# Performance work log

Measured on AMD Instinct MI355X. Metric: run time of the kernel, lower is better.

The kernel has to match this reference:

```python
import jax, jax.numpy as jnp
import numpy as np
import math

D_MODEL = 1024
NUM_HEADS = 16
D_K = D_MODEL // NUM_HEADS
THETA = 10000.0
NEG_INF = 1.0e6  # module uses -1e6, not -inf


def _rope_tables(seq_len):
    pair_idx = jnp.arange(0, D_K, 2, dtype=jnp.float32)
    inv_freq = 1.0 / (THETA ** (pair_idx / D_K))
    pos = jnp.arange(seq_len, dtype=jnp.float32)
    angles = jnp.outer(pos, inv_freq)  # (S, D_K//2)
    return jnp.cos(angles), jnp.sin(angles)


def _apply_rope(x, cos, sin):
    # x: (B, H, S, D_K); cos/sin: (S, D_K//2)
    xe = x[..., 0::2]
    xo = x[..., 1::2]
    oe = xe * cos - xo * sin
    oo = xe * sin + xo * cos
    return jnp.stack([oe, oo], axis=-1).reshape(x.shape)


def setup_inputs() -> dict:
    key = jax.random.key(0)
    k0, k1, k2, k3, k4 = jax.random.split(key, 5)
    B, S = 2, 2048
    x = jax.random.normal(k0, (B, S, D_MODEL), dtype=jnp.float32)
    scale = 0.02
    wq = jax.random.normal(k1, (D_MODEL, D_MODEL), dtype=jnp.float32) * scale
    wk = jax.random.normal(k2, (D_MODEL, D_MODEL), dtype=jnp.float32) * scale
    wv = jax.random.normal(k3, (D_MODEL, D_MODEL), dtype=jnp.float32) * scale
    wo = jax.random.normal(k4, (D_MODEL, D_MODEL), dtype=jnp.float32) * scale
    return {"x": x, "wq": wq, "wk": wk, "wv": wv, "wo": wo}


def reference(x, wq, wk, wv, wo):
    B, S, _ = x.shape
    q = x @ wq.T
    k = x @ wk.T
    v = x @ wv.T
    # (B, S, H, d_k) -> (B, H, S, d_k)
    q = q.reshape(B, S, NUM_HEADS, D_K).transpose(0, 2, 1, 3)
    k = k.reshape(B, S, NUM_HEADS, D_K).transpose(0, 2, 1, 3)
    v = v.reshape(B, S, NUM_HEADS, D_K).transpose(0, 2, 1, 3)
    cos, sin = _rope_tables(S)
    q = _apply_rope(q, cos, sin)
    k = _apply_rope(k, cos, sin)
    scores = jnp.einsum("bhqd,bhkd->bhqk", q, k) / math.sqrt(D_K)
    causal = jnp.tril(jnp.ones((S, S), dtype=bool))
    scores = jnp.where(causal, scores, -NEG_INF)
    attn = jax.nn.softmax(scores, axis=-1)
    out = jnp.einsum("bhqk,bhkd->bhqd", attn, v)
    out = out.transpose(0, 2, 1, 3).reshape(B, S, D_MODEL)
    return out @ wo.T
```

## Files before the change

### kernel.cpp

```cpp
#include <hip/hip_runtime.h>

typedef __attribute__((ext_vector_type(8))) __bf16 bf16x8;
typedef __attribute__((ext_vector_type(8))) _Float16 f16x8;
typedef __attribute__((ext_vector_type(4))) _Float16 f16x4;
typedef __attribute__((ext_vector_type(4))) float f32x4;
typedef __attribute__((ext_vector_type(8))) unsigned short u16x8;
typedef __attribute__((ext_vector_type(4))) unsigned int u32x4;

#define MFMA_BF16(a, b, c) __builtin_amdgcn_mfma_f32_16x16x32_bf16((a), (b), (c), 0, 0, 0)
#define MFMA_F16(a, b, c)  __builtin_amdgcn_mfma_f32_16x16x32_f16((a), (b), (c), 0, 0, 0)
#define LOG2E 1.44269504088896340736f
#define QSCALE 0.18033688011112042f

__device__ __forceinline__ float b2f(unsigned short u) {
    union { unsigned int i; float f; } v; v.i = ((unsigned int)u) << 16; return v.f;
}
__device__ __forceinline__ unsigned short f2bf(float f) {
    union { float f; unsigned int i; } v; v.f = f;
    unsigned int u = v.i;
    return (unsigned short)((u + 0x7fffu + ((u >> 16) & 1u)) >> 16);
}

__device__ __forceinline__ void gl_lds16(const void* g, void* l) {
    __builtin_amdgcn_global_load_lds(
        (const __attribute__((address_space(1))) void*)g,
        (__attribute__((address_space(3))) void*)l,
        16, 0, 0);
}

__global__ __launch_bounds__(256) void cvt_all(const float* __restrict__ x,
                                               const float* __restrict__ wq,
                                               const float* __restrict__ wk,
                                               const float* __restrict__ wv,
                                               const float* __restrict__ wo,
                                               unsigned short* __restrict__ xb,
                                               unsigned short* __restrict__ wqb,
                                               unsigned short* __restrict__ wkb,
                                               unsigned short* __restrict__ wvb,
                                               unsigned short* __restrict__ wob) {
    int id = blockIdx.x * 256 + threadIdx.x;
    const float* src; unsigned short* dst; size_t off; float scl = 1.0f;
    if (id < 524288)      { src = x;  dst = xb;  off = (size_t)id * 8; }
    else if (id < 655360) { src = wq; dst = wqb; off = (size_t)(id - 524288) * 8; scl = QSCALE; }
    else if (id < 786432) { src = wk; dst = wkb; off = (size_t)(id - 655360) * 8; }
    else if (id < 917504) { src = wv; dst = wvb; off = (size_t)(id - 786432) * 8; }
    else                  { src = wo; dst = wob; off = (size_t)(id - 917504) * 8; }
    float4 a = *(const float4*)(src + off);
    float4 b = *(const float4*)(src + off + 4);
    u16x8 o;
    o[0] = f2bf(a.x * scl); o[1] = f2bf(a.y * scl); o[2] = f2bf(a.z * scl); o[3] = f2bf(a.w * scl);
    o[4] = f2bf(b.x * scl); o[5] = f2bf(b.y * scl); o[6] = f2bf(b.z * scl); o[7] = f2bf(b.w * scl);
    *(u16x8*)(dst + off) = o;
}

template <int MODE>
__device__ __forceinline__ void gemm128_bt(const unsigned short* __restrict__ A,
                                           const unsigned short* __restrict__ B,
                                           void* __restrict__ Cv,
                                           int m0, int n0, int ldc,
                                           unsigned short* As, unsigned short* Bs) {
    const int tid = threadIdx.x;
    const int w = tid >> 6, lane = tid & 63;
    const int quad = lane >> 4, l15 = lane & 15;
    const int wm = w & 1, wn = w >> 1;

    f32x4 acc[4][4];
#pragma unroll
    for (int mt = 0; mt < 4; ++mt)
#pragma unroll
        for (int nt = 0; nt < 4; ++nt) acc[mt][nt] = f32x4{0.f, 0.f, 0.f, 0.f};

    for (int k0 = 0; k0 < 1024; k0 += 32) {
        __syncthreads();
#pragma unroll
        for (int i = 0; i < 2; ++i) {
            int L = (w * 2 + i) * 64 + lane;
            int r = L >> 2;
            int c = (L & 3) ^ ((r >> 1) & 3);
            gl_lds16(A + (size_t)(m0 + r) * 1024 + k0 + c * 8, As + L * 8);
            gl_lds16(B + (size_t)(n0 + r) * 1024 + k0 + c * 8, Bs + L * 8);
        }
        __syncthreads();

        bf16x8 af[4], bfr[4];
#pragma unroll
        for (int mt = 0; mt < 4; ++mt) {
            int row = wm * 64 + mt * 16 + l15;
            af[mt] = *(const bf16x8*)(As + row * 32 + (quad ^ ((row >> 1) & 3)) * 8);
        }
#pragma unroll
        for (int nt = 0; nt < 4; ++nt) {
            int row = wn * 64 + nt * 16 + l15;
            bfr[nt] = *(const bf16x8*)(Bs + row * 32 + (quad ^ ((row >> 1) & 3)) * 8);
        }
#pragma unroll
        for (int mt = 0; mt < 4; ++mt)
#pragma unroll
            for (int nt = 0; nt < 4; ++nt)
                acc[mt][nt] = MFMA_BF16(af[mt], bfr[nt], acc[mt][nt]);
    }

    float invf[4], sgn = 0.f;
    if constexpr (MODE == 3) {
        sgn = (l15 & 1) ? 1.0f : -1.0f;
#pragma unroll
        for (int nt = 0; nt < 4; ++nt)
            invf[nt] = exp2f(-0.41524101186092029f * (float)((nt * 16 + l15) >> 1));
    }

#pragma unroll
    for (int mt = 0; mt < 4; ++mt) {
        int grow = m0 + wm * 64 + mt * 16 + quad * 4;
#pragma unroll
        for (int nt = 0; nt < 4; ++nt) {
            int gcol = n0 + wn * 64 + nt * 16 + l15;
#pragma unroll
            for (int r = 0; r < 4; ++r) {
                float val = acc[mt][nt][r];
                size_t idx = (size_t)(grow + r) * ldc + gcol;
                if constexpr (MODE == 0) {
                    ((unsigned short*)Cv)[idx] = f2bf(val);
                } else if constexpr (MODE == 1) {
                    ((float*)Cv)[idx] = val;
                } else if constexpr (MODE == 2) {
                    _Float16 hv = (_Float16)val;
                    ((unsigned short*)Cv)[idx] = __builtin_bit_cast(unsigned short, hv);
                } else {
                    float p = __shfl_xor(val, 1);
                    float pos = (float)((grow + r) & 2047);
                    float ang = pos * invf[nt];
                    float out = val * __cosf(ang) + sgn * p * __sinf(ang);
                    ((unsigned short*)Cv)[idx] = f2bf(out);
                }
            }
        }
    }
}

__global__ __launch_bounds__(256) void gemm_qkv(const unsigned short* __restrict__ X,
                                                const unsigned short* __restrict__ Wq,
                                                const unsigned short* __restrict__ Wk,
                                                const unsigned short* __restrict__ Wv,
                                                unsigned short* __restrict__ Qo,
                                                unsigned short* __restrict__ Ko,
                                                unsigned short* __restrict__ Vt) {
    __shared__ unsigned short As[128 * 32];
    __shared__ unsigned short Bs[128 * 32];
    int y = blockIdx.y;
    if (y < 16) {
        int sel = y >> 3;
        int m0 = blockIdx.x * 128;
        int n0 = (y & 7) * 128;
        const unsigned short* B = sel ? Wk : Wq;
        unsigned short* C = sel ? Ko : Qo;
        gemm128_bt<3>(X, B, C, m0, n0, 1024, As, Bs);
    } else {
        int m0 = (y & 7) * 128;
        int n0 = blockIdx.x * 128;
        gemm128_bt<2>(Wv, X, Vt, m0, n0, 4096, As, Bs);
    }
}

__global__ __launch_bounds__(256) void gemm_out(const unsigned short* __restrict__ A,
                                                const unsigned short* __restrict__ Wo,
                                                float* __restrict__ C) {
    __shared__ unsigned short As[128 * 32];
    __shared__ unsigned short Bs[128 * 32];
    gemm128_bt<1>(A, Wo, C, blockIdx.x * 128, blockIdx.y * 128, 1024, As, Bs);
}

#define FBODY(MASKED)                                                                   \
    {                                                                                   \
        bf16x8 kf[4][2];                                                                \
        _Pragma("unroll")                                                               \
        for (int nt = 0; nt < 4; ++nt) {                                                \
            int row = nt * 16 + l15;                                                    \
            const char* kp = (const char*)Ksb + row * 128;                              \
            int swk = row & 7;                                                          \
            kf[nt][0] = *(const bf16x8*)(kp + ((quad ^ swk) << 4));                     \
            kf[nt][1] = *(const bf16x8*)(kp + (((quad ^ 4) ^ swk) << 4));               \
        }                                                                               \
        f16x8 pf[2][2];                                                                 \
        _Pragma("unroll")                                                               \
        for (int mt = 0; mt < 2; ++mt) {                                                \
            f32x4 sc[4];                                                                \
            _Pragma("unroll")                                                           \
            for (int nt = 0; nt < 4; ++nt) {                                            \
                f32x4 z = f32x4{0.f, 0.f, 0.f, 0.f};                                    \
                z = MFMA_BF16(kf[nt][0], qf[mt][0], z);                                 \
                sc[nt] = MFMA_BF16(kf[nt][1], qf[mt][1], z);                            \
            }                                                                           \
            int qpos = qposw + mt * 16 + l15;                                           \
            unsigned pk[8];                                                             \
            _Pragma("unroll")                                                           \
            for (int nt = 0; nt < 4; ++nt) {                                            \
                float e[4];                                                             \
                _Pragma("unroll")                                                       \
                for (int r = 0; r < 4; ++r) {                                           \
                    float ev = exp2f(sc[nt][r]);                                        \
                    if (MASKED) {                                                       \
                        int kpos = kb * 64 + nt * 16 + quad * 4 + r;                    \
                        ev = (kpos > qpos) ? 0.f : ev;                                  \
                    }                                                                   \
                    e[r] = ev;                                                          \
                }                                                                       \
                pk[nt * 2 + 0] = __builtin_bit_cast(unsigned,                           \
                                     __builtin_amdgcn_cvt_pkrtz(e[0], e[1]));           \
                pk[nt * 2 + 1] = __builtin_bit_cast(unsigned,                           \
                                     __builtin_amdgcn_cvt_pkrtz(e[2], e[3]));           \
            }                                                                           \
            u32x4 pw0 = u32x4{pk[0], pk[1], pk[2], pk[3]};                              \
            u32x4 pw1 = u32x4{pk[4], pk[5], pk[6], pk[7]};                              \
            pf[mt][0] = __builtin_bit_cast(f16x8, pw0);                                 \
            pf[mt][1] = __builtin_bit_cast(f16x8, pw1);                                 \
            lacc[mt] = MFMA_F16(pf[mt][0], ones, lacc[mt]);                             \
            lacc[mt] = MFMA_F16(pf[mt][1], ones, lacc[mt]);                             \
        }                                                                               \
        _Pragma("unroll")                                                               \
        for (int nt = 0; nt < 4; ++nt) {                                                \
            int rowd = nt * 16 + l15;                                                   \
            const char* vp = (const char*)Vsb + rowd * 128;                             \
            int swv = rowd & 7;                                                         \
            int qh = quad >> 1, sub = (quad & 1) * 8;                                   \
            f16x4 a0 = *(const f16x4*)(vp + (((qh + 0) ^ swv) << 4) + sub);             \
            f16x4 a1 = *(const f16x4*)(vp + (((qh + 2) ^ swv) << 4) + sub);             \
            f16x8 v0 = __builtin_shufflevector(a0, a1, 0, 1, 2, 3, 4, 5, 6, 7);         \
            accO[0][nt] = MFMA_F16(pf[0][0], v0, accO[0][nt]);                          \
            accO[1][nt] = MFMA_F16(pf[1][0], v0, accO[1][nt]);                          \
            f16x4 b0 = *(const f16x4*)(vp + (((qh + 4) ^ swv) << 4) + sub);             \
            f16x4 b1 = *(const f16x4*)(vp + (((qh + 6) ^ swv) << 4) + sub);             \
            f16x8 v1 = __builtin_shufflevector(b0, b1, 0, 1, 2, 3, 4, 5, 6, 7);         \
            accO[0][nt] = MFMA_F16(pf[0][1], v1, accO[0][nt]);                          \
            accO[1][nt] = MFMA_F16(pf[1][1], v1, accO[1][nt]);                          \
        }                                                                               \
    }

__global__ __launch_bounds__(256) void flash_attn(const unsigned short* __restrict__ Q,
                                                  const unsigned short* __restrict__ Kb,
                                                  const unsigned short* __restrict__ Vt,
                                                  unsigned short* __restrict__ O) {
    int id = blockIdx.x;
    int xcd = id & 7;
    int sl = id >> 3;
    int rr = sl >> 3;
    int j  = sl & 7;
    int bh = xcd + 8 * rr;
    int b = bh >> 4, h = bh & 15;
    int tid = threadIdx.x, w = tid >> 6, lane = tid & 63;
    int quad = lane >> 4, l15 = lane & 15;

    __shared__ unsigned short Ks[2 * 4096];
    __shared__ unsigned short Vs[2 * 4096];

    int L0 = w * 128 + lane;
    int L1 = L0 + 64;
    int r0 = L0 >> 3, c0 = (L0 & 7) ^ (r0 & 7);
    int r1 = L1 >> 3, c1 = (L1 & 7) ^ (r1 & 7);
    const unsigned short* Kg0 = Kb + (size_t)(b * 2048 + r0) * 1024 + h * 64 + c0 * 8;
    const unsigned short* Kg1 = Kb + (size_t)(b * 2048 + r1) * 1024 + h * 64 + c1 * 8;
    const unsigned short* Vg0 = Vt + (size_t)(h * 64 + r0) * 4096 + b * 2048 + c0 * 8;
    const unsigned short* Vg1 = Vt + (size_t)(h * 64 + r1) * 4096 + b * 2048 + c1 * 8;

    f16x8 ones;
#pragma unroll
    for (int t = 0; t < 8; ++t) ones[t] = (_Float16)1.0f;

#define STAGE(kb_, buf_)                                                    \
    {                                                                       \
        size_t ko = (size_t)(kb_) * 64 * 1024;                              \
        size_t vo = (size_t)(kb_) * 64;                                     \
        unsigned short* kd = Ks + (buf_) * 4096;                            \
        unsigned short* vd = Vs + (buf_) * 4096;                            \
        gl_lds16(Kg0 + ko, kd + L0 * 8);                                    \
        gl_lds16(Kg1 + ko, kd + L1 * 8);                                    \
        gl_lds16(Vg0 + vo, vd + L0 * 8);                                    \
        gl_lds16(Vg1 + vo, vd + L1 * 8);                                    \
    }

    for (int tp = 0; tp < 2; ++tp) {
        int qt = tp ? (15 - j) : j;
        int qrow0 = b * 2048 + qt * 128 + w * 32;
        int qposw = qt * 128 + w * 32;
        int nkb = 2 * qt + 2;

        STAGE(0, 0)

        bf16x8 qf[2][2];
#pragma unroll
        for (int mt = 0; mt < 2; ++mt) {
            const unsigned short* qp =
                Q + (size_t)(qrow0 + mt * 16 + l15) * 1024 + h * 64 + quad * 8;
            qf[mt][0] = *(const bf16x8*)qp;
            qf[mt][1] = *(const bf16x8*)(qp + 32);
        }

        f32x4 accO[2][4];
        f32x4 lacc[2];
#pragma unroll
        for (int mt = 0; mt < 2; ++mt) {
            lacc[mt] = f32x4{0.f, 0.f, 0.f, 0.f};
#pragma unroll
            for (int nt = 0; nt < 4; ++nt) accO[mt][nt] = f32x4{0.f, 0.f, 0.f, 0.f};
        }

        __asm__ volatile("s_waitcnt vmcnt(0)" ::: "memory");
        __builtin_amdgcn_s_barrier();
        __builtin_amdgcn_sched_barrier(0);

        int cur = 0;
        for (int kb = 0; kb < nkb; ++kb) {
            if (kb + 1 < nkb) STAGE(kb + 1, cur ^ 1)
            const unsigned short* Ksb = Ks + cur * 4096;
            const unsigned short* Vsb = Vs + cur * 4096;
            if (kb < nkb - 2) {
                FBODY(0)
            } else {
                FBODY(1)
            }
            __asm__ volatile("s_waitcnt vmcnt(0)" ::: "memory");
            __builtin_amdgcn_s_barrier();
            __builtin_amdgcn_sched_barrier(0);
            cur ^= 1;
        }

#pragma unroll
        for (int mt = 0; mt < 2; ++mt) {
            float inv[4];
#pragma unroll
            for (int r = 0; r < 4; ++r) inv[r] = 1.0f / lacc[mt][r];
#pragma unroll
            for (int nt = 0; nt < 4; ++nt)
#pragma unroll
                for (int r = 0; r < 4; ++r)
                    O[(size_t)(qrow0 + mt * 16 + quad * 4 + r) * 1024 +
                      h * 64 + nt * 16 + l15] = f2bf(accO[mt][nt][r] * inv[r]);
        }
    }
#undef STAGE
}

extern "C" void kernel_launch(void* const* d_in, const int* in_sizes, int n_in,
                              void* d_out, int out_size, void* d_ws, size_t ws_size,
                              hipStream_t stream) {
    (void)in_sizes; (void)n_in; (void)out_size; (void)ws_size;
    const float* x  = (const float*)d_in[0];
    const float* wq = (const float*)d_in[1];
    const float* wk = (const float*)d_in[2];
    const float* wv = (const float*)d_in[3];
    const float* wo = (const float*)d_in[4];
    float* out = (float*)d_out;

    const size_t T = (size_t)4096 * 1024;
    const size_t W = (size_t)1024 * 1024;
    unsigned short* Q   = (unsigned short*)d_ws;
    unsigned short* K   = Q + T;
    unsigned short* Vt  = K + T;
    unsigned short* xb  = Vt + T;
    unsigned short* AO  = xb;
    unsigned short* wqb = xb + T;
    unsigned short* wkb = wqb + W;
    unsigned short* wvb = wkb + W;
    unsigned short* wob = wvb + W;

    cvt_all  <<<dim3(4096),   256, 0, stream>>>(x, wq, wk, wv, wo, xb, wqb, wkb, wvb, wob);
    gemm_qkv <<<dim3(32, 24), 256, 0, stream>>>(xb, wqb, wkb, wvb, Q, K, Vt);
    flash_attn<<<dim3(256),   256, 0, stream>>>(Q, K, Vt, AO);
    gemm_out <<<dim3(32, 8),  256, 0, stream>>>(AO, wob, out);
}
```

Baseline: 187.4 us.

## Split flash attention into one q-tile per block and swizzle P fragments

The attention kernel previously had each of 256 blocks process two paired query tiles (j and 15-j) one after another. It now launches 512 blocks, each handling a single query tile, with a causal-balanced ordering mapping t to qt. This is meant to improve occupancy and tail balance across CUs. Separately, the P operand is rearranged across lanes using ds_swizzle, so V fragments can be read from LDS as single 16-byte loads instead of two 8-byte loads plus a shuffle. The cost is extra swizzle instructions and more blocks, each with its own prologue and Q load.

```diff
diff --git a/kernel.cpp b/kernel.cpp
--- a/kernel.cpp
+++ b/kernel.cpp
@@ -2,7 +2,6 @@
 
 typedef __attribute__((ext_vector_type(8))) __bf16 bf16x8;
 typedef __attribute__((ext_vector_type(8))) _Float16 f16x8;
-typedef __attribute__((ext_vector_type(4))) _Float16 f16x4;
 typedef __attribute__((ext_vector_type(4))) float f32x4;
 typedef __attribute__((ext_vector_type(8))) unsigned short u16x8;
 typedef __attribute__((ext_vector_type(4))) unsigned int u32x4;
@@ -175,12 +174,12 @@
         _Pragma("unroll")                                                               \
         for (int nt = 0; nt < 4; ++nt) {                                                \
             int row = nt * 16 + l15;                                                    \
-            const char* kp = (const char*)Ksb + row * 128;                              \
+            const unsigned short* kp = Ksb + row * 64;                                  \
             int swk = row & 7;                                                          \
-            kf[nt][0] = *(const bf16x8*)(kp + ((quad ^ swk) << 4));                     \
-            kf[nt][1] = *(const bf16x8*)(kp + (((quad ^ 4) ^ swk) << 4));               \
+            kf[nt][0] = *(const bf16x8*)(kp + (quad ^ swk) * 8);                        \
+            kf[nt][1] = *(const bf16x8*)(kp + ((quad ^ 4) ^ swk) * 8);                  \
         }                                                                               \
-        f16x8 pf[2][2];                                                                 \
+        f16x8 pa[2][2];                                                                 \
         _Pragma("unroll")                                                               \
         for (int mt = 0; mt < 2; ++mt) {                                                \
             f32x4 sc[4];                                                                \
@@ -209,29 +208,37 @@
                 pk[nt * 2 + 1] = __builtin_bit_cast(unsigned,                           \
                                      __builtin_amdgcn_cvt_pkrtz(e[2], e[3]));           \
             }                                                                           \
-            u32x4 pw0 = u32x4{pk[0], pk[1], pk[2], pk[3]};                              \
-            u32x4 pw1 = u32x4{pk[4], pk[5], pk[6], pk[7]};                              \
-            pf[mt][0] = __builtin_bit_cast(f16x8, pw0);                                 \
-            pf[mt][1] = __builtin_bit_cast(f16x8, pw1);                                 \
-            lacc[mt] = MFMA_F16(pf[mt][0], ones, lacc[mt]);                             \
-            lacc[mt] = MFMA_F16(pf[mt][1], ones, lacc[mt]);                             \
+            u32x4 rs0 = u32x4{pk[0], pk[1], pk[2], pk[3]};                              \
+            u32x4 rs1 = u32x4{pk[4], pk[5], pk[6], pk[7]};                              \
+            lacc[mt] = MFMA_F16(__builtin_bit_cast(f16x8, rs0), ones, lacc[mt]);        \
+            lacc[mt] = MFMA_F16(__builtin_bit_cast(f16x8, rs1), ones, lacc[mt]);        \
+            int b0 = quad & 1;                                                          \
+            unsigned y0 = (unsigned)__builtin_amdgcn_ds_swizzle(                        \
+                              (int)(b0 ? pk[0] : pk[2]), 0x401F);                       \
+            unsigned y1 = (unsigned)__builtin_amdgcn_ds_swizzle(                        \
+                              (int)(b0 ? pk[1] : pk[3]), 0x401F);                       \
+            unsigned y2 = (unsigned)__builtin_amdgcn_ds_swizzle(                        \
+                              (int)(b0 ? pk[4] : pk[6]), 0x401F);                       \
+            unsigned y3 = (unsigned)__builtin_amdgcn_ds_swizzle(                        \
+                              (int)(b0 ? pk[5] : pk[7]), 0x401F);                       \
+            u32x4 t0 = b0 ? u32x4{y0, y1, pk[2], pk[3]}                                 \
+                          : u32x4{pk[0], pk[1], y0, y1};                                \
+            u32x4 t1 = b0 ? u32x4{y2, y3, pk[6], pk[7]}                                 \
+                          : u32x4{pk[4], pk[5], y2, y3};                                \
+            pa[mt][0] = __builtin_bit_cast(f16x8, t0);                                  \
+            pa[mt][1] = __builtin_bit_cast(f16x8, t1);                                  \
         }                                                                               \
         _Pragma("unroll")                                                               \
         for (int nt = 0; nt < 4; ++nt) {                                                \
             int rowd = nt * 16 + l15;                                                   \
-            const char* vp = (const char*)Vsb + rowd * 128;                             \
-            int swv = rowd & 7;                                                         \
-            int qh = quad >> 1, sub = (quad & 1) * 8;                                   \
-            f16x4 a0 = *(const f16x4*)(vp + (((qh + 0) ^ swv) << 4) + sub);             \
-            f16x4 a1 = *(const f16x4*)(vp + (((qh + 2) ^ swv) << 4) + sub);             \
-            f16x8 v0 = __builtin_shufflevector(a0, a1, 0, 1, 2, 3, 4, 5, 6, 7);         \
-            accO[0][nt] = MFMA_F16(pf[0][0], v0, accO[0][nt]);                          \
-            accO[1][nt] = MFMA_F16(pf[1][0], v0, accO[1][nt]);                          \
-            f16x4 b0 = *(const f16x4*)(vp + (((qh + 4) ^ swv) << 4) + sub);             \
-            f16x4 b1 = *(const f16x4*)(vp + (((qh + 6) ^ swv) << 4) + sub);             \
-            f16x8 v1 = __builtin_shufflevector(b0, b1, 0, 1, 2, 3, 4, 5, 6, 7);         \
-            accO[0][nt] = MFMA_F16(pf[0][1], v1, accO[0][nt]);                          \
-            accO[1][nt] = MFMA_F16(pf[1][1], v1, accO[1][nt]);                          \
+            const unsigned short* vp = Vsb + rowd * 64;                                 \
+            int sl0 = pi4 ^ (rowd & 7);                                                 \
+            f16x8 v0 = *(const f16x8*)(vp + sl0 * 8);                                   \
+            f16x8 v1 = *(const f16x8*)(vp + (sl0 ^ 4) * 8);                             \
+            accO[0][nt] = MFMA_F16(pa[0][0], v0, accO[0][nt]);                          \
+            accO[1][nt] = MFMA_F16(pa[1][0], v0, accO[1][nt]);                          \
+            accO[0][nt] = MFMA_F16(pa[0][1], v1, accO[0][nt]);                          \
+            accO[1][nt] = MFMA_F16(pa[1][1], v1, accO[1][nt]);                          \
         }                                                                               \
     }
 
@@ -241,13 +248,15 @@
                                                   unsigned short* __restrict__ O) {
     int id = blockIdx.x;
     int xcd = id & 7;
-    int sl = id >> 3;
-    int rr = sl >> 3;
-    int j  = sl & 7;
+    int s  = id >> 3;
+    int rr = s & 3;
+    int t  = s >> 2;
+    int qt = (t < 8) ? t : 23 - t;
     int bh = xcd + 8 * rr;
     int b = bh >> 4, h = bh & 15;
     int tid = threadIdx.x, w = tid >> 6, lane = tid & 63;
     int quad = lane >> 4, l15 = lane & 15;
+    int pi4 = ((quad & 1) << 1) | (quad >> 1);
 
     __shared__ unsigned short Ks[2 * 4096];
     __shared__ unsigned short Vs[2 * 4096];
@@ -263,7 +272,7 @@
 
     f16x8 ones;
 #pragma unroll
-    for (int t = 0; t < 8; ++t) ones[t] = (_Float16)1.0f;
+    for (int tt = 0; tt < 8; ++tt) ones[tt] = (_Float16)1.0f;
 
 #define STAGE(kb_, buf_)                                                    \
     {                                                                       \
@@ -277,64 +286,61 @@
         gl_lds16(Vg1 + vo, vd + L1 * 8);                                    \
     }
 
-    for (int tp = 0; tp < 2; ++tp) {
-        int qt = tp ? (15 - j) : j;
-        int qrow0 = b * 2048 + qt * 128 + w * 32;
-        int qposw = qt * 128 + w * 32;
-        int nkb = 2 * qt + 2;
-
-        STAGE(0, 0)
-
-        bf16x8 qf[2][2];
-#pragma unroll
-        for (int mt = 0; mt < 2; ++mt) {
-            const unsigned short* qp =
-                Q + (size_t)(qrow0 + mt * 16 + l15) * 1024 + h * 64 + quad * 8;
-            qf[mt][0] = *(const bf16x8*)qp;
-            qf[mt][1] = *(const bf16x8*)(qp + 32);
-        }
-
-        f32x4 accO[2][4];
-        f32x4 lacc[2];
-#pragma unroll
-        for (int mt = 0; mt < 2; ++mt) {
-            lacc[mt] = f32x4{0.f, 0.f, 0.f, 0.f};
-#pragma unroll
-            for (int nt = 0; nt < 4; ++nt) accO[mt][nt] = f32x4{0.f, 0.f, 0.f, 0.f};
-        }
-
+    int qrow0 = b * 2048 + qt * 128 + w * 32;
+    int qposw = qt * 128 + w * 32;
+    int nkb = 2 * qt + 2;
+
+    STAGE(0, 0)
+
+    bf16x8 qf[2][2];
+#pragma unroll
+    for (int mt = 0; mt < 2; ++mt) {
+        const unsigned short* qp =
+            Q + (size_t)(qrow0 + mt * 16 + l15) * 1024 + h * 64 + quad * 8;
+        qf[mt][0] = *(const bf16x8*)qp;
+        qf[mt][1] = *(const bf16x8*)(qp + 32);
+    }
+
+    f32x4 accO[2][4];
+    f32x4 lacc[2];
+#pragma unroll
+    for (int mt = 0; mt < 2; ++mt) {
+        lacc[mt] = f32x4{0.f, 0.f, 0.f, 0.f};
+#pragma unroll
+        for (int nt = 0; nt < 4; ++nt) accO[mt][nt] = f32x4{0.f, 0.f, 0.f, 0.f};
+    }
+
+    __asm__ volatile("s_waitcnt vmcnt(0)" ::: "memory");
+    __builtin_amdgcn_s_barrier();
+    __builtin_amdgcn_sched_barrier(0);
+
+    int cur = 0;
+    for (int kb = 0; kb < nkb; ++kb) {
+        if (kb + 1 < nkb) STAGE(kb + 1, cur ^ 1)
+        const unsigned short* Ksb = Ks + cur * 4096;
+        const unsigned short* Vsb = Vs + cur * 4096;
+        if (kb < nkb - 2) {
+            FBODY(0)
+        } else {
+            FBODY(1)
+        }
         __asm__ volatile("s_waitcnt vmcnt(0)" ::: "memory");
         __builtin_amdgcn_s_barrier();
         __builtin_amdgcn_sched_barrier(0);
-
-        int cur = 0;
-        for (int kb = 0; kb < nkb; ++kb) {
-            if (kb + 1 < nkb) STAGE(kb + 1, cur ^ 1)
-            const unsigned short* Ksb = Ks + cur * 4096;
-            const unsigned short* Vsb = Vs + cur * 4096;
-            if (kb < nkb - 2) {
-                FBODY(0)
-            } else {
-                FBODY(1)
-            }
-            __asm__ volatile("s_waitcnt vmcnt(0)" ::: "memory");
-            __builtin_amdgcn_s_barrier();
-            __builtin_amdgcn_sched_barrier(0);
-            cur ^= 1;
-        }
-
-#pragma unroll
-        for (int mt = 0; mt < 2; ++mt) {
-            float inv[4];
-#pragma unroll
-            for (int r = 0; r < 4; ++r) inv[r] = 1.0f / lacc[mt][r];
-#pragma unroll
-            for (int nt = 0; nt < 4; ++nt)
-#pragma unroll
-                for (int r = 0; r < 4; ++r)
-                    O[(size_t)(qrow0 + mt * 16 + quad * 4 + r) * 1024 +
-                      h * 64 + nt * 16 + l15] = f2bf(accO[mt][nt][r] * inv[r]);
-        }
+        cur ^= 1;
+    }
+
+#pragma unroll
+    for (int mt = 0; mt < 2; ++mt) {
+        float inv[4];
+#pragma unroll
+        for (int r = 0; r < 4; ++r) inv[r] = 1.0f / lacc[mt][r];
+#pragma unroll
+        for (int nt = 0; nt < 4; ++nt)
+#pragma unroll
+            for (int r = 0; r < 4; ++r)
+                O[(size_t)(qrow0 + mt * 16 + quad * 4 + r) * 1024 +
+                  h * 64 + nt * 16 + l15] = f2bf(accO[mt][nt][r] * inv[r]);
     }
 #undef STAGE
 }
@@ -364,6 +370,6 @@
 
     cvt_all  <<<dim3(4096),   256, 0, stream>>>(x, wq, wk, wv, wo, xb, wqb, wkb, wvb, wob);
     gemm_qkv <<<dim3(32, 24), 256, 0, stream>>>(xb, wqb, wkb, wvb, Q, K, Vt);
-    flash_attn<<<dim3(256),   256, 0, stream>>>(Q, K, Vt, AO);
+    flash_attn<<<dim3(512),   256, 0, stream>>>(Q, K, Vt, AO);
     gemm_out <<<dim3(32, 8),  256, 0, stream>>>(AO, wob, out);
 }
```

New measurement: 190.5 us. About the same (+1.7%).

## Load K/V directly into registers with single-wave blocks in flash attention

Applied to the files above, without the earlier changes.

Rewrites the attention kernel so that each 64-thread block handles one 32-row query slice. K and V fragments are loaded straight from global memory into registers with a two-deep software prefetch, replacing the LDS staging, the barriers and the paired causal-tile scheduling. Blocks are ordered so the longest query tiles launch first. The change removes LDS traffic and synchronization, but the global K/V reads are no longer shared across the waves of a block, so L2 and global bandwidth demand rises and register pressure grows.

```diff
diff --git a/kernel.cpp b/kernel.cpp
--- a/kernel.cpp
+++ b/kernel.cpp
@@ -169,26 +169,43 @@
     gemm128_bt<1>(A, Wo, C, blockIdx.x * 128, blockIdx.y * 128, 1024, As, Bs);
 }
 
-#define FBODY(MASKED)                                                                   \
+
+#define LOADK(DST, KB_)                                                     \
+    {                                                                       \
+        const unsigned short* kp_ = KgL + (size_t)(KB_) * 65536;            \
+        DST[0][0] = *(const bf16x8*)(kp_);                                  \
+        DST[0][1] = *(const bf16x8*)(kp_ + 32);                             \
+        DST[1][0] = *(const bf16x8*)(kp_ + 16384);                          \
+        DST[1][1] = *(const bf16x8*)(kp_ + 16384 + 32);                     \
+        DST[2][0] = *(const bf16x8*)(kp_ + 32768);                          \
+        DST[2][1] = *(const bf16x8*)(kp_ + 32768 + 32);                     \
+        DST[3][0] = *(const bf16x8*)(kp_ + 49152);                          \
+        DST[3][1] = *(const bf16x8*)(kp_ + 49152 + 32);                     \
+    }
+
+#define LOADV(DST, KB_)                                                     \
+    {                                                                       \
+        const unsigned short* vp_ = VgL + (size_t)(KB_) * 64;               \
+        _Pragma("unroll")                                                   \
+        for (int nt_ = 0; nt_ < 4; ++nt_) {                                 \
+            DST[nt_][0] = *(const f16x4*)(vp_ + nt_ * 65536);               \
+            DST[nt_][1] = *(const f16x4*)(vp_ + nt_ * 65536 + 16);          \
+            DST[nt_][2] = *(const f16x4*)(vp_ + nt_ * 65536 + 32);          \
+            DST[nt_][3] = *(const f16x4*)(vp_ + nt_ * 65536 + 48);          \
+        }                                                                   \
+    }
+
+#define FCOMP(KF, VP, KB_, MASKED)                                                      \
     {                                                                                   \
-        bf16x8 kf[4][2];                                                                \
-        _Pragma("unroll")                                                               \
-        for (int nt = 0; nt < 4; ++nt) {                                                \
-            int row = nt * 16 + l15;                                                    \
-            const char* kp = (const char*)Ksb + row * 128;                              \
-            int swk = row & 7;                                                          \
-            kf[nt][0] = *(const bf16x8*)(kp + ((quad ^ swk) << 4));                     \
-            kf[nt][1] = *(const bf16x8*)(kp + (((quad ^ 4) ^ swk) << 4));               \
-        }                                                                               \
-        f16x8 pf[2][2];                                                                 \
+        f16x8 paR[2][2];                                                                \
         _Pragma("unroll")                                                               \
         for (int mt = 0; mt < 2; ++mt) {                                                \
             f32x4 sc[4];                                                                \
             _Pragma("unroll")                                                           \
             for (int nt = 0; nt < 4; ++nt) {                                            \
                 f32x4 z = f32x4{0.f, 0.f, 0.f, 0.f};                                    \
-                z = MFMA_BF16(kf[nt][0], qf[mt][0], z);                                 \
-                sc[nt] = MFMA_BF16(kf[nt][1], qf[mt][1], z);                            \
+                z = MFMA_BF16(KF[nt][0], qf[mt][0], z);                                 \
+                sc[nt] = MFMA_BF16(KF[nt][1], qf[mt][1], z);                            \
             }                                                                           \
             int qpos = qposw + mt * 16 + l15;                                           \
             unsigned pk[8];                                                             \
@@ -199,7 +216,7 @@
                 for (int r = 0; r < 4; ++r) {                                           \
                     float ev = exp2f(sc[nt][r]);                                        \
                     if (MASKED) {                                                       \
-                        int kpos = kb * 64 + nt * 16 + quad * 4 + r;                    \
+                        int kpos = (KB_) * 64 + nt * 16 + quad * 4 + r;                 \
                         ev = (kpos > qpos) ? 0.f : ev;                                  \
                     }                                                                   \
                     e[r] = ev;                                                          \
@@ -209,134 +226,104 @@
                 pk[nt * 2 + 1] = __builtin_bit_cast(unsigned,                           \
                                      __builtin_amdgcn_cvt_pkrtz(e[2], e[3]));           \
             }                                                                           \
-            u32x4 pw0 = u32x4{pk[0], pk[1], pk[2], pk[3]};                              \
-            u32x4 pw1 = u32x4{pk[4], pk[5], pk[6], pk[7]};                              \
-            pf[mt][0] = __builtin_bit_cast(f16x8, pw0);                                 \
-            pf[mt][1] = __builtin_bit_cast(f16x8, pw1);                                 \
-            lacc[mt] = MFMA_F16(pf[mt][0], ones, lacc[mt]);                             \
-            lacc[mt] = MFMA_F16(pf[mt][1], ones, lacc[mt]);                             \
+            u32x4 w0 = u32x4{pk[0], pk[1], pk[2], pk[3]};                               \
+            u32x4 w1 = u32x4{pk[4], pk[5], pk[6], pk[7]};                               \
+            f16x8 pa0 = __builtin_bit_cast(f16x8, w0);                                  \
+            f16x8 pa1 = __builtin_bit_cast(f16x8, w1);                                  \
+            lacc[mt] = MFMA_F16(pa0, ones, lacc[mt]);                                   \
+            lacc[mt] = MFMA_F16(pa1, ones, lacc[mt]);                                   \
+            paR[mt][0] = pa0;                                                           \
+            paR[mt][1] = pa1;                                                           \
         }                                                                               \
         _Pragma("unroll")                                                               \
         for (int nt = 0; nt < 4; ++nt) {                                                \
-            int rowd = nt * 16 + l15;                                                   \
-            const char* vp = (const char*)Vsb + rowd * 128;                             \
-            int swv = rowd & 7;                                                         \
-            int qh = quad >> 1, sub = (quad & 1) * 8;                                   \
-            f16x4 a0 = *(const f16x4*)(vp + (((qh + 0) ^ swv) << 4) + sub);             \
-            f16x4 a1 = *(const f16x4*)(vp + (((qh + 2) ^ swv) << 4) + sub);             \
-            f16x8 v0 = __builtin_shufflevector(a0, a1, 0, 1, 2, 3, 4, 5, 6, 7);         \
-            accO[0][nt] = MFMA_F16(pf[0][0], v0, accO[0][nt]);                          \
-            accO[1][nt] = MFMA_F16(pf[1][0], v0, accO[1][nt]);                          \
-            f16x4 b0 = *(const f16x4*)(vp + (((qh + 4) ^ swv) << 4) + sub);             \
-            f16x4 b1 = *(const f16x4*)(vp + (((qh + 6) ^ swv) << 4) + sub);             \
-            f16x8 v1 = __builtin_shufflevector(b0, b1, 0, 1, 2, 3, 4, 5, 6, 7);         \
-            accO[0][nt] = MFMA_F16(pf[0][1], v1, accO[0][nt]);                          \
-            accO[1][nt] = MFMA_F16(pf[1][1], v1, accO[1][nt]);                          \
+            f16x8 v0 = __builtin_shufflevector(VP[nt][0], VP[nt][1],                    \
+                                               0, 1, 2, 3, 4, 5, 6, 7);                 \
+            f16x8 v1 = __builtin_shufflevector(VP[nt][2], VP[nt][3],                    \
+                                               0, 1, 2, 3, 4, 5, 6, 7);                 \
+            accO[0][nt] = MFMA_F16(paR[0][0], v0, accO[0][nt]);                         \
+            accO[1][nt] = MFMA_F16(paR[1][0], v0, accO[1][nt]);                         \
+            accO[0][nt] = MFMA_F16(paR[0][1], v1, accO[0][nt]);                         \
+            accO[1][nt] = MFMA_F16(paR[1][1], v1, accO[1][nt]);                         \
         }                                                                               \
     }
 
-__global__ __launch_bounds__(256) void flash_attn(const unsigned short* __restrict__ Q,
-                                                  const unsigned short* __restrict__ Kb,
-                                                  const unsigned short* __restrict__ Vt,
-                                                  unsigned short* __restrict__ O) {
+__global__ __launch_bounds__(64, 2) void flash_attn(const unsigned short* __restrict__ Q,
+                                                    const unsigned short* __restrict__ Kb,
+                                                    const unsigned short* __restrict__ Vt,
+                                                    unsigned short* __restrict__ O) {
     int id = blockIdx.x;
     int xcd = id & 7;
-    int sl = id >> 3;
-    int rr = sl >> 3;
-    int j  = sl & 7;
+    int idx = id >> 3;
+    int rr = idx & 3;
+    int w  = (idx >> 2) & 3;
+    int qt = 15 - (idx >> 4);
     int bh = xcd + 8 * rr;
     int b = bh >> 4, h = bh & 15;
-    int tid = threadIdx.x, w = tid >> 6, lane = tid & 63;
+    int lane = threadIdx.x & 63;
     int quad = lane >> 4, l15 = lane & 15;
 
-    __shared__ unsigned short Ks[2 * 4096];
-    __shared__ unsigned short Vs[2 * 4096];
-
-    int L0 = w * 128 + lane;
-    int L1 = L0 + 64;
-    int r0 = L0 >> 3, c0 = (L0 & 7) ^ (r0 & 7);
-    int r1 = L1 >> 3, c1 = (L1 & 7) ^ (r1 & 7);
-    const unsigned short* Kg0 = Kb + (size_t)(b * 2048 + r0) * 1024 + h * 64 + c0 * 8;
-    const unsigned short* Kg1 = Kb + (size_t)(b * 2048 + r1) * 1024 + h * 64 + c1 * 8;
-    const unsigned short* Vg0 = Vt + (size_t)(h * 64 + r0) * 4096 + b * 2048 + c0 * 8;
-    const unsigned short* Vg1 = Vt + (size_t)(h * 64 + r1) * 4096 + b * 2048 + c1 * 8;
+    int qrow0 = b * 2048 + qt * 128 + w * 32;
+    int qposw = qt * 128 + w * 32;
+    int nkb = 2 * qt + 2;
+
+    const unsigned short* KgL = Kb + (size_t)(b * 2048 + l15) * 1024 + h * 64 + quad * 8;
+    const unsigned short* VgL = Vt + (size_t)(h * 64 + l15) * 4096 + b * 2048 + quad * 4;
+
+    bf16x8 qf[2][2];
+#pragma unroll
+    for (int mt = 0; mt < 2; ++mt) {
+        const unsigned short* qp =
+            Q + (size_t)(qrow0 + mt * 16 + l15) * 1024 + h * 64 + quad * 8;
+        qf[mt][0] = *(const bf16x8*)qp;
+        qf[mt][1] = *(const bf16x8*)(qp + 32);
+    }
 
     f16x8 ones;
 #pragma unroll
-    for (int t = 0; t < 8; ++t) ones[t] = (_Float16)1.0f;
-
-#define STAGE(kb_, buf_)                                                    \
-    {                                                                       \
-        size_t ko = (size_t)(kb_) * 64 * 1024;                              \
-        size_t vo = (size_t)(kb_) * 64;                                     \
-        unsigned short* kd = Ks + (buf_) * 4096;                            \
-        unsigned short* vd = Vs + (buf_) * 4096;                            \
-        gl_lds16(Kg0 + ko, kd + L0 * 8);                                    \
-        gl_lds16(Kg1 + ko, kd + L1 * 8);                                    \
-        gl_lds16(Vg0 + vo, vd + L0 * 8);                                    \
-        gl_lds16(Vg1 + vo, vd + L1 * 8);                                    \
-    }
-
-    for (int tp = 0; tp < 2; ++tp) {
-        int qt = tp ? (15 - j) : j;
-        int qrow0 = b * 2048 + qt * 128 + w * 32;
-        int qposw = qt * 128 + w * 32;
-        int nkb = 2 * qt + 2;
-
-        STAGE(0, 0)
-
-        bf16x8 qf[2][2];
-#pragma unroll
-        for (int mt = 0; mt < 2; ++mt) {
-            const unsigned short* qp =
-                Q + (size_t)(qrow0 + mt * 16 + l15) * 1024 + h * 64 + quad * 8;
-            qf[mt][0] = *(const bf16x8*)qp;
-            qf[mt][1] = *(const bf16x8*)(qp + 32);
-        }
-
-        f32x4 accO[2][4];
-        f32x4 lacc[2];
-#pragma unroll
-        for (int mt = 0; mt < 2; ++mt) {
-            lacc[mt] = f32x4{0.f, 0.f, 0.f, 0.f};
-#pragma unroll
-            for (int nt = 0; nt < 4; ++nt) accO[mt][nt] = f32x4{0.f, 0.f, 0.f, 0.f};
-        }
-
-        __asm__ volatile("s_waitcnt vmcnt(0)" ::: "memory");
-        __builtin_amdgcn_s_barrier();
-        __builtin_amdgcn_sched_barrier(0);
-
-        int cur = 0;
-        for (int kb = 0; kb < nkb; ++kb) {
-            if (kb + 1 < nkb) STAGE(kb + 1, cur ^ 1)
-            const unsigned short* Ksb = Ks + cur * 4096;
-            const unsigned short* Vsb = Vs + cur * 4096;
-            if (kb < nkb - 2) {
-                FBODY(0)
-            } else {
-                FBODY(1)
-            }
-            __asm__ volatile("s_waitcnt vmcnt(0)" ::: "memory");
-            __builtin_amdgcn_s_barrier();
-            __builtin_amdgcn_sched_barrier(0);
-            cur ^= 1;
-        }
-
-#pragma unroll
-        for (int mt = 0; mt < 2; ++mt) {
-            float inv[4];
-#pragma unroll
-            for (int r = 0; r < 4; ++r) inv[r] = 1.0f / lacc[mt][r];
-#pragma unroll
-            for (int nt = 0; nt < 4; ++nt)
-#pragma unroll
-                for (int r = 0; r < 4; ++r)
-                    O[(size_t)(qrow0 + mt * 16 + quad * 4 + r) * 1024 +
-                      h * 64 + nt * 16 + l15] = f2bf(accO[mt][nt][r] * inv[r]);
-        }
-    }
-#undef STAGE
+    for (int tt = 0; tt < 8; ++tt) ones[tt] = (_Float16)1.0f;
+
+    f32x4 accO[2][4];
+    f32x4 lacc[2];
+#pragma unroll
+    for (int mt = 0; mt < 2; ++mt) {
+        lacc[mt] = f32x4{0.f, 0.f, 0.f, 0.f};
+#pragma unroll
+        for (int nt = 0; nt < 4; ++nt) accO[mt][nt] = f32x4{0.f, 0.f, 0.f, 0.f};
+    }
+
+    bf16x8 kA[4][2], kB[4][2];
+    f16x4 vA[4][4], vB[4][4];
+
+    LOADK(kA, 0)
+
+    int kb = 0;
+    for (; kb < nkb - 2; kb += 2) {
+        LOADV(vA, kb)
+        LOADK(kB, kb + 1)
+        FCOMP(kA, vA, kb, 0)
+        LOADV(vB, kb + 1)
+        LOADK(kA, kb + 2)
+        FCOMP(kB, vB, kb + 1, 0)
+    }
+    LOADV(vA, kb)
+    LOADK(kB, kb + 1)
+    FCOMP(kA, vA, kb, 1)
+    LOADV(vB, kb + 1)
+    FCOMP(kB, vB, kb + 1, 1)
+
+#pragma unroll
+    for (int mt = 0; mt < 2; ++mt) {
+        float inv[4];
+#pragma unroll
+        for (int r = 0; r < 4; ++r) inv[r] = 1.0f / lacc[mt][r];
+#pragma unroll
+        for (int nt = 0; nt < 4; ++nt)
+#pragma unroll
+            for (int r = 0; r < 4; ++r)
+                O[(size_t)(qrow0 + mt * 16 + quad * 4 + r) * 1024 +
+                  h * 64 + nt * 16 + l15] = f2bf(accO[mt][nt][r] * inv[r]);
+    }
 }
 
 extern "C" void kernel_launch(void* const* d_in, const int* in_sizes, int n_in,
@@ -364,6 +351,6 @@
 
     cvt_all  <<<dim3(4096),   256, 0, stream>>>(x, wq, wk, wv, wo, xb, wqb, wkb, wvb, wob);
     gemm_qkv <<<dim3(32, 24), 256, 0, stream>>>(xb, wqb, wkb, wvb, Q, K, Vt);
-    flash_attn<<<dim3(256),   256, 0, stream>>>(Q, K, Vt, AO);
+    flash_attn<<<dim3(2048),  64,  0, stream>>>(Q, K, Vt, AO);
     gemm_out <<<dim3(32, 8),  256, 0, stream>>>(AO, wob, out);
 }
```

After: 238.4 us. 1.27x slower.
